# Optimization experiments

Hardware: AMD Instinct MI355X
Metric: run time of the kernel (lower is better)

The kernel has to match this reference:

```python
import jax, jax.numpy as jnp
import numpy as np

N_NODES = 50000
N_EDGES = 800000
NUM_GRAPHS = 256
F_IN = 64        # num_features (per-head out dim == in dim in this module)
HEADS = 4        # n_heads1
OUT_DIM = 128    # output_dim
HC = HEADS * F_IN
NEG_SLOPE = 0.2  # GATConv leaky_relu slope
EPS = 1e-5       # GraphNorm eps


def setup_inputs() -> dict:
    key = jax.random.key(0)
    ks = jax.random.split(key, 12)
    s = lambda k, shape, fan: (jax.random.normal(k, shape, jnp.float32) / np.sqrt(fan).astype(np.float32))
    return {
        "x": jax.random.normal(ks[0], (N_NODES, F_IN), jnp.float32),
        "edge_index": jax.random.randint(ks[1], (2, N_EDGES), 0, N_NODES),
        "batch": jnp.sort(jax.random.randint(ks[2], (N_NODES,), 0, NUM_GRAPHS)),
        # GATConv params
        "lin_w": s(ks[3], (HC, F_IN), F_IN),
        "att_src": s(ks[4], (HEADS, F_IN), F_IN),
        "att_dst": s(ks[5], (HEADS, F_IN), F_IN),
        "gat_bias": jnp.zeros((HC,), jnp.float32),
        # GraphNorm params
        "gn_weight": jnp.ones((HC,), jnp.float32),
        "gn_bias": jnp.zeros((HC,), jnp.float32),
        "gn_mean_scale": jnp.ones((HC,), jnp.float32),
        # fc_g1 / out heads
        "fc1_w": s(ks[6], (OUT_DIM, HC), HC), "fc1_b": jnp.zeros((OUT_DIM,), jnp.float32),
        "out_w": s(ks[7], (1, OUT_DIM), OUT_DIM), "out_b": jnp.zeros((1,), jnp.float32),
        # GlobalAttention gate_nn: Linear(HC,16) -> ReLU -> Linear(16,1) -> Sigmoid
        "att1_w": s(ks[8], (16, HC), HC), "att1_b": jnp.zeros((16,), jnp.float32),
        "att2_w": s(ks[9], (1, 16), 16), "att2_b": jnp.zeros((1,), jnp.float32),
    }


def _gat_conv(x, edge_index, lin_w, att_src, att_dst, gat_bias):
    """PyG GATConv with add_self_loops=True, concat heads. Returns (out [N,HC], alpha [E+N,H])."""
    N = x.shape[0]
    xh = (x @ lin_w.T).reshape(N, HEADS, F_IN)                 # [N,H,C]
    a_src = (xh * att_src[None]).sum(-1)                        # [N,H]
    a_dst = (xh * att_dst[None]).sum(-1)                        # [N,H]
    loops = jnp.arange(N)
    src = jnp.concatenate([edge_index[0], loops])               # [E+N]
    dst = jnp.concatenate([edge_index[1], loops])
    alpha = jax.nn.leaky_relu(a_src[src] + a_dst[dst], NEG_SLOPE)  # [E+N,H]
    # segment softmax over incoming edges of each dst node (self-loops guarantee non-empty)
    amax = jax.ops.segment_max(alpha, dst, num_segments=N)
    alpha = jnp.exp(alpha - amax[dst])
    denom = jax.ops.segment_sum(alpha, dst, num_segments=N)
    alpha = alpha / (denom[dst] + 1e-16)
    msg = xh[src] * alpha[:, :, None]                           # [E+N,H,C]
    out = jax.ops.segment_sum(msg, dst, num_segments=N).reshape(N, HC) + gat_bias
    return out, alpha


def _graph_norm(x, batch, weight, bias, mean_scale):
    ones = jnp.ones((x.shape[0],), x.dtype)
    cnt = jnp.maximum(jax.ops.segment_sum(ones, batch, num_segments=NUM_GRAPHS), 1.0)[:, None]
    mean = jax.ops.segment_sum(x, batch, num_segments=NUM_GRAPHS) / cnt
    sub = x - mean[batch] * mean_scale
    var = jax.ops.segment_sum(sub * sub, batch, num_segments=NUM_GRAPHS) / cnt
    return weight * sub / jnp.sqrt(var + EPS)[batch] + bias


def _global_attention(x, batch, att1_w, att1_b, att2_w, att2_b):
    gate = jax.nn.sigmoid(jax.nn.relu(x @ att1_w.T + att1_b) @ att2_w.T + att2_b)  # [N,1]
    gmax = jax.ops.segment_max(gate, batch, num_segments=NUM_GRAPHS)
    gate = jnp.exp(gate - gmax[batch])
    gden = jax.ops.segment_sum(gate, batch, num_segments=NUM_GRAPHS)
    gate = gate / (gden[batch] + 1e-16)
    return jax.ops.segment_sum(gate * x, batch, num_segments=NUM_GRAPHS)  # [G,HC]


def reference(x, edge_index, batch, lin_w, att_src, att_dst, gat_bias,
              gn_weight, gn_bias, gn_mean_scale, fc1_w, fc1_b, out_w, out_b,
              att1_w, att1_b, att2_w, att2_b):
    x2, alpha = _gat_conv(x, edge_index, lin_w, att_src, att_dst, gat_bias)
    h = _graph_norm(x2, batch, gn_weight, gn_bias, gn_mean_scale)
    h = jax.nn.relu(h)                                # node_dropout = identity (eval)
    pooled = _global_attention(h, batch, att1_w, att1_b, att2_w, att2_b)
    h = jax.nn.relu(pooled @ fc1_w.T + fc1_b)          # dropout = identity (eval)
    out = jax.nn.sigmoid(h @ out_w.T + out_b)          # [G,1]
    return out, alpha
```

## Files before the change

kernel.cpp:

```cpp
#include <hip/hip_runtime.h>
#include <hip/hip_fp16.h>
#include <math.h>

#define NN 50000
#define NE 800000
#define NG 256
#define NEG_SLOPE 0.2f
#define GEPS 1e-5f
#define CHUNK 64
#define NB 196
#define CAP 6144
#define NAB 196
#define EPB 4096
#define SPLIT 8
#define NLINB 782
#define ABLK 3321
#define GMAX 512

typedef _Float16 f16x8 __attribute__((ext_vector_type(8)));
typedef _Float16 f16x4 __attribute__((ext_vector_type(4)));
typedef float f32x4 __attribute__((ext_vector_type(4)));
typedef float f32x2 __attribute__((ext_vector_type(2)));

__device__ __forceinline__ float lrelu(float v){ return v > 0.f ? v : NEG_SLOPE * v; }

__global__ __launch_bounds__(256) void k_misc(const float* __restrict__ lin_w,
                                              _Float16* __restrict__ wh,
                                              const float* __restrict__ att1_w,
                                              _Float16* __restrict__ a1w,
                                              const int* __restrict__ batch,
                                              int* __restrict__ goff,
                                              int* __restrict__ gcnt,
                                              int* __restrict__ bucket_cnt) {
  int b = blockIdx.x, tid = threadIdx.x;
  if (b == 0) {
    if (tid < NB) bucket_cnt[tid] = 0;
    int g = tid;
    int lo = 0, hi = NN;
    while (lo < hi) { int mid = (lo + hi) >> 1; if (batch[mid] < g) lo = mid + 1; else hi = mid; }
    int start = lo;
    lo = 0; hi = NN;
    while (lo < hi) { int mid = (lo + hi) >> 1; if (batch[mid] < g + 1) lo = mid + 1; else hi = mid; }
    goff[g] = start;
    gcnt[g] = lo - start;
  } else if (b <= 16) {
    int i0 = (b - 1) * 1024 + tid * 4;
    float4 f = *(const float4*)&lin_w[i0];
    f16x4 h4;
    h4[0] = (_Float16)f.x; h4[1] = (_Float16)f.y; h4[2] = (_Float16)f.z; h4[3] = (_Float16)f.w;
    *(f16x4*)&wh[i0] = h4;
  } else {
    int i0 = (b - 17) * 1024 + tid * 4;
    float4 f = *(const float4*)&att1_w[i0];
    f16x4 h4;
    h4[0] = (_Float16)f.x; h4[1] = (_Float16)f.y; h4[2] = (_Float16)f.z; h4[3] = (_Float16)f.w;
    *(f16x4*)&a1w[i0] = h4;
  }
}

__device__ __forceinline__ void lin_body(char* smem,
                                         const float* __restrict__ x,
                                         const _Float16* __restrict__ wh,
                                         const float* __restrict__ att_src,
                                         const float* __restrict__ att_dst,
                                         unsigned char* __restrict__ xh8,
                                         float* __restrict__ a_src_n,
                                         float* __restrict__ a_dst_n) {
  unsigned char* s_f8 = (unsigned char*)smem;
  int w = threadIdx.x >> 6, lane = threadIdx.x & 63;
  int nb = blockIdx.x * 64 + w * 16;
  if (nb >= NN) return;
  int am = lane & 15, quad = lane >> 4;
  int wb = w * 4096;

  const float* xr = x + (size_t)(nb + am) * 64 + quad * 8;
  float4 f0 = *(const float4*)(xr);
  float4 f1 = *(const float4*)(xr + 4);
  float4 f2 = *(const float4*)(xr + 32);
  float4 f3 = *(const float4*)(xr + 36);
  f16x8 a0, a1;
  a0[0] = (_Float16)f0.x; a0[1] = (_Float16)f0.y; a0[2] = (_Float16)f0.z; a0[3] = (_Float16)f0.w;
  a0[4] = (_Float16)f1.x; a0[5] = (_Float16)f1.y; a0[6] = (_Float16)f1.z; a0[7] = (_Float16)f1.w;
  a1[0] = (_Float16)f2.x; a1[1] = (_Float16)f2.y; a1[2] = (_Float16)f2.z; a1[3] = (_Float16)f2.w;
  a1[4] = (_Float16)f3.x; a1[5] = (_Float16)f3.y; a1[6] = (_Float16)f3.z; a1[7] = (_Float16)f3.w;

  f32x4 acc[16];
#pragma unroll
  for (int ct = 0; ct < 16; ct++) acc[ct] = (f32x4){0.f, 0.f, 0.f, 0.f};

#pragma unroll
  for (int ct = 0; ct < 16; ct++) {
    const _Float16* wbp = wh + (size_t)(ct * 16 + am) * 64 + quad * 8;
    f16x8 b0 = *(const f16x8*)(wbp);
    f16x8 b1 = *(const f16x8*)(wbp + 32);
    acc[ct] = __builtin_amdgcn_mfma_f32_16x16x32_f16(a0, b0, acc[ct], 0, 0, 0);
    acc[ct] = __builtin_amdgcn_mfma_f32_16x16x32_f16(a1, b1, acc[ct], 0, 0, 0);
  }

  float ps[4][4], pd[4][4];
#pragma unroll
  for (int r = 0; r < 4; r++)
#pragma unroll
    for (int h = 0; h < 4; h++) { ps[r][h] = 0.f; pd[r][h] = 0.f; }
#pragma unroll
  for (int ct = 0; ct < 16; ct++) {
    int c = ct * 16 + am;
    float av = att_src[c];
    float dv = att_dst[c];
    int h = ct >> 2;
#pragma unroll
    for (int r = 0; r < 4; r++) {
      float v = acc[ct][r];
      ps[r][h] += v * av;
      pd[r][h] += v * dv;
    }
  }
#pragma unroll
  for (int r = 0; r < 4; r++)
#pragma unroll
    for (int h = 0; h < 4; h++) {
      float s = ps[r][h], d = pd[r][h];
#pragma unroll
      for (int o = 1; o < 16; o <<= 1) {
        s += __shfl_xor(s, o, 64);
        d += __shfl_xor(d, o, 64);
      }
      if (am == 0) {
        int node = nb + quad * 4 + r;
        a_src_n[node * 4 + h] = s;
        a_dst_n[node * 4 + h] = d;
      }
    }

#pragma unroll
  for (int r = 0; r < 4; r++) {
    uint4 u;
    int t;
    t = __builtin_amdgcn_cvt_pk_fp8_f32(acc[0][r],  acc[1][r],  0, 0);
    t = __builtin_amdgcn_cvt_pk_fp8_f32(acc[2][r],  acc[3][r],  t, 1);
    u.x = (unsigned)t;
    t = __builtin_amdgcn_cvt_pk_fp8_f32(acc[4][r],  acc[5][r],  0, 0);
    t = __builtin_amdgcn_cvt_pk_fp8_f32(acc[6][r],  acc[7][r],  t, 1);
    u.y = (unsigned)t;
    t = __builtin_amdgcn_cvt_pk_fp8_f32(acc[8][r],  acc[9][r],  0, 0);
    t = __builtin_amdgcn_cvt_pk_fp8_f32(acc[10][r], acc[11][r], t, 1);
    u.z = (unsigned)t;
    t = __builtin_amdgcn_cvt_pk_fp8_f32(acc[12][r], acc[13][r], 0, 0);
    t = __builtin_amdgcn_cvt_pk_fp8_f32(acc[14][r], acc[15][r], t, 1);
    u.w = (unsigned)t;
    *(uint4*)&s_f8[wb + (quad * 4 + r) * 256 + am * 16] = u;
  }
#pragma unroll
  for (int p = 0; p < 4; p++) {
    uint4 u = *(const uint4*)&s_f8[wb + p * 1024 + lane * 16];
    *(uint4*)&xh8[(size_t)nb * 256 + p * 1024 + lane * 16] = u;
  }
}

__device__ __forceinline__ void binA_body(char* smem, int b,
                                          const int* __restrict__ ei,
                                          int* __restrict__ bucket_cnt,
                                          int2* __restrict__ ebuf) {
  int2* sorted = (int2*)smem;
  int*  hist   = (int*)(smem + 32768);
  int*  lbase  = (int*)(smem + 33552);
  int*  cur    = (int*)(smem + 34336);
  int*  runb   = (int*)(smem + 35120);
  int*  wsum   = (int*)(smem + 35904);
  int tid = threadIdx.x, lane = tid & 63, wid = tid >> 6;
  int e0 = b * EPB, e1 = min(e0 + EPB, NE);
  int n = e1 - e0;
  bool full = (e0 + EPB <= NE);

  int dd[16];
  if (full) {
#pragma unroll
    for (int r = 0; r < 4; r++) {
      int e = e0 + r * 1024 + tid * 4;
      int4 v = *(const int4*)&ei[NE + e];
      dd[r * 4 + 0] = v.x; dd[r * 4 + 1] = v.y;
      dd[r * 4 + 2] = v.z; dd[r * 4 + 3] = v.w;
    }
  } else {
#pragma unroll
    for (int r = 0; r < 4; r++)
#pragma unroll
      for (int k = 0; k < 4; k++) {
        int e = e0 + r * 1024 + tid * 4 + k;
        dd[r * 4 + k] = (e < e1) ? ei[NE + e] : -1;
      }
  }
  for (int i = tid; i < NB; i += 256) hist[i] = 0;
  __syncthreads();
#pragma unroll
  for (int q = 0; q < 16; q++)
    if (dd[q] >= 0) atomicAdd(&hist[dd[q] >> 8], 1);
  __syncthreads();
  {
    int v = (tid < NB) ? hist[tid] : 0;
    int s = v;
#pragma unroll
    for (int o = 1; o < 64; o <<= 1) { int t = __shfl_up(s, o, 64); if (lane >= o) s += t; }
    if (lane == 63) wsum[wid] = s;
    __syncthreads();
    int wbase = 0;
    for (int k = 0; k < wid; k++) wbase += wsum[k];
    if (tid < NB) {
      int ex = wbase + s - v;
      lbase[tid] = ex;
      cur[tid] = ex;
      runb[tid] = atomicAdd(&bucket_cnt[tid], v);
    }
  }
  __syncthreads();
  int ss[16];
  if (full) {
#pragma unroll
    for (int r = 0; r < 4; r++) {
      int e = e0 + r * 1024 + tid * 4;
      int4 v = *(const int4*)&ei[e];
      ss[r * 4 + 0] = v.x; ss[r * 4 + 1] = v.y;
      ss[r * 4 + 2] = v.z; ss[r * 4 + 3] = v.w;
    }
  } else {
#pragma unroll
    for (int r = 0; r < 4; r++)
#pragma unroll
      for (int k = 0; k < 4; k++) {
        int e = e0 + r * 1024 + tid * 4 + k;
        ss[r * 4 + k] = (e < e1) ? ei[e] : 0;
      }
  }
#pragma unroll
  for (int q = 0; q < 16; q++) {
    int d = dd[q];
    if (d >= 0) {
      int lp = atomicAdd(&cur[d >> 8], 1);
      sorted[lp] = make_int2(d, ss[q]);
    }
  }
  __syncthreads();
  for (int i = tid; i < n; i += 256) {
    int2 e = sorted[i];
    int bk = e.x >> 8;
    int slot = runb[bk] + (i - lbase[bk]);
    if (slot < CAP) ebuf[(size_t)bk * CAP + slot] = e;
  }
}

__global__ __launch_bounds__(256) void k_linbin(const float* __restrict__ x,
                                                const _Float16* __restrict__ wh,
                                                const float* __restrict__ att_src,
                                                const float* __restrict__ att_dst,
                                                unsigned char* __restrict__ xh8,
                                                float* __restrict__ a_src_n,
                                                float* __restrict__ a_dst_n,
                                                const int* __restrict__ ei,
                                                int* __restrict__ bucket_cnt,
                                                int2* __restrict__ ebuf) {
  __shared__ __align__(16) char smem[35920];
  if (blockIdx.x < NLINB)
    lin_body(smem, x, wh, att_src, att_dst, xh8, a_src_n, a_dst_n);
  else
    binA_body(smem, blockIdx.x - NLINB, ei, bucket_cnt, ebuf);
}

__global__ __launch_bounds__(256) void k_binB(const int2* __restrict__ ebuf,
                                              const int* __restrict__ bucket_cnt,
                                              int* __restrict__ deg,
                                              int* __restrict__ offs,
                                              int* __restrict__ src_list) {
  __shared__ int hist[256];
  __shared__ int cur[256];
  __shared__ int wsum[4];
  __shared__ int bbase[NB];
  int b = blockIdx.x, tid = threadIdx.x, lane = tid & 63, wid = tid >> 6;
  {
    int v = (tid < NB) ? min(bucket_cnt[tid], CAP) : 0;
    int s = v;
#pragma unroll
    for (int o = 1; o < 64; o <<= 1) { int t = __shfl_up(s, o, 64); if (lane >= o) s += t; }
    if (lane == 63) wsum[wid] = s;
    __syncthreads();
    int wbase = 0;
    for (int k = 0; k < wid; k++) wbase += wsum[k];
    if (tid < NB) bbase[tid] = wbase + s - v;
  }
  __syncthreads();
  int cnt = min(bucket_cnt[b], CAP);
  int base = bbase[b];
  const int2* seg = ebuf + (size_t)b * CAP;
  hist[tid] = 0;
  __syncthreads();
  for (int i = tid; i < cnt; i += 256) atomicAdd(&hist[seg[i].x & 255], 1);
  __syncthreads();
  int v = hist[tid];
  int s = v;
#pragma unroll
  for (int o = 1; o < 64; o <<= 1) { int t = __shfl_up(s, o, 64); if (lane >= o) s += t; }
  if (lane == 63) wsum[wid] = s;
  __syncthreads();
  int wbase = 0;
  for (int k = 0; k < wid; k++) wbase += wsum[k];
  int excl = wbase + s - v;
  int node = b * 256 + tid;
  if (node < NN) {
    deg[node] = v;
    offs[node] = base + excl;
  }
  cur[tid] = excl;
  __syncthreads();
  for (int i = tid; i < cnt; i += 256) {
    int2 e = seg[i];
    int pos = base + atomicAdd(&cur[e.x & 255], 1);
    src_list[pos] = e.y;
  }
}

__global__ __launch_bounds__(64) void k_gat(const unsigned char* __restrict__ xh8,
                                            const float* __restrict__ a_src_n,
                                            const float* __restrict__ a_dst_n,
                                            const int* __restrict__ offs,
                                            const int* __restrict__ deg_arr,
                                            const int* __restrict__ src_list,
                                            const float* __restrict__ gat_bias,
                                            __half* __restrict__ x2h,
                                            float* __restrict__ den_inv) {
  __shared__ __align__(16) float s_al[CHUNK * 4];
  __shared__ int s_src[CHUNK];
  __shared__ __half s_tr[256];
  int n = blockIdx.x, lane = threadIdx.x;
  int off = offs[n], dg = deg_arr[n], cnt = dg + 1;
  float4 ad = *(const float4*)&a_dst_n[n * 4];
  int h = lane & 3;
  unsigned loff = 4u * (unsigned)lane;
  float acc0 = 0.f, acc1 = 0.f, acc2 = 0.f, acc3 = 0.f;

  if (cnt <= 64) {
    float e0 = 0.f, e1 = 0.f, e2 = 0.f, e3 = 0.f;
    if (lane < cnt) {
      int src = (lane < dg) ? src_list[off + lane] : n;
      float4 as = *(const float4*)&a_src_n[src * 4];
      e0 = __expf(lrelu(as.x + ad.x));
      e1 = __expf(lrelu(as.y + ad.y));
      e2 = __expf(lrelu(as.z + ad.z));
      e3 = __expf(lrelu(as.w + ad.w));
      s_src[lane] = src;
    }
    float s0 = e0, s1 = e1, s2 = e2, s3 = e3;
#pragma unroll
    for (int o = 32; o >= 1; o >>= 1) {
      s0 += __shfl_xor(s0, o, 64);
      s1 += __shfl_xor(s1, o, 64);
      s2 += __shfl_xor(s2, o, 64);
      s3 += __shfl_xor(s3, o, 64);
    }
    float i0 = 1.f / (s0 + 1e-16f), i1 = 1.f / (s1 + 1e-16f);
    float i2 = 1.f / (s2 + 1e-16f), i3 = 1.f / (s3 + 1e-16f);
    if (lane == 0) *(float4*)&den_inv[n * 4] = make_float4(i0, i1, i2, i3);
    if (lane < cnt) {
      s_al[lane * 4 + 0] = e0 * i0;
      s_al[lane * 4 + 1] = e1 * i1;
      s_al[lane * 4 + 2] = e2 * i2;
      s_al[lane * 4 + 3] = e3 * i3;
    }
    __syncthreads();
    int j = 0;
    for (; j + 4 <= cnt; j += 4) {
      unsigned oA = ((unsigned)s_src[j] << 8) + loff;
      unsigned oB = ((unsigned)s_src[j + 1] << 8) + loff;
      unsigned oC = ((unsigned)s_src[j + 2] << 8) + loff;
      unsigned oD = ((unsigned)s_src[j + 3] << 8) + loff;
      unsigned rA = *(const unsigned*)&xh8[oA];
      unsigned rB = *(const unsigned*)&xh8[oB];
      unsigned rC = *(const unsigned*)&xh8[oC];
      unsigned rD = *(const unsigned*)&xh8[oD];
      float aA = s_al[j * 4 + h], aB = s_al[(j + 1) * 4 + h];
      float aC = s_al[(j + 2) * 4 + h], aD = s_al[(j + 3) * 4 + h];
      f32x2 lA = __builtin_amdgcn_cvt_pk_f32_fp8((int)rA, 0);
      f32x2 hA = __builtin_amdgcn_cvt_pk_f32_fp8((int)rA, 1);
      f32x2 lB = __builtin_amdgcn_cvt_pk_f32_fp8((int)rB, 0);
      f32x2 hB = __builtin_amdgcn_cvt_pk_f32_fp8((int)rB, 1);
      f32x2 lC = __builtin_amdgcn_cvt_pk_f32_fp8((int)rC, 0);
      f32x2 hC = __builtin_amdgcn_cvt_pk_f32_fp8((int)rC, 1);
      f32x2 lD = __builtin_amdgcn_cvt_pk_f32_fp8((int)rD, 0);
      f32x2 hD = __builtin_amdgcn_cvt_pk_f32_fp8((int)rD, 1);
      acc0 += aA * lA[0] + aB * lB[0] + aC * lC[0] + aD * lD[0];
      acc1 += aA * lA[1] + aB * lB[1] + aC * lC[1] + aD * lD[1];
      acc2 += aA * hA[0] + aB * hB[0] + aC * hC[0] + aD * hD[0];
      acc3 += aA * hA[1] + aB * hB[1] + aC * hC[1] + aD * hD[1];
    }
    for (; j < cnt; j++) {
      unsigned oA = ((unsigned)s_src[j] << 8) + loff;
      unsigned rA = *(const unsigned*)&xh8[oA];
      float aA = s_al[j * 4 + h];
      f32x2 lA = __builtin_amdgcn_cvt_pk_f32_fp8((int)rA, 0);
      f32x2 hA = __builtin_amdgcn_cvt_pk_f32_fp8((int)rA, 1);
      acc0 += aA * lA[0];
      acc1 += aA * lA[1];
      acc2 += aA * hA[0];
      acc3 += aA * hA[1];
    }
  } else {
    float s0 = 0.f, s1 = 0.f, s2 = 0.f, s3 = 0.f;
    for (int j = lane; j < cnt; j += 64) {
      int src = (j < dg) ? src_list[off + j] : n;
      float4 as = *(const float4*)&a_src_n[src * 4];
      s0 += __expf(lrelu(as.x + ad.x));
      s1 += __expf(lrelu(as.y + ad.y));
      s2 += __expf(lrelu(as.z + ad.z));
      s3 += __expf(lrelu(as.w + ad.w));
    }
#pragma unroll
    for (int o = 32; o >= 1; o >>= 1) {
      s0 += __shfl_xor(s0, o, 64);
      s1 += __shfl_xor(s1, o, 64);
      s2 += __shfl_xor(s2, o, 64);
      s3 += __shfl_xor(s3, o, 64);
    }
    float i0 = 1.f / (s0 + 1e-16f), i1 = 1.f / (s1 + 1e-16f);
    float i2 = 1.f / (s2 + 1e-16f), i3 = 1.f / (s3 + 1e-16f);
    if (lane == 0) *(float4*)&den_inv[n * 4] = make_float4(i0, i1, i2, i3);
    for (int cb = 0; cb < cnt; cb += CHUNK) {
      int clen = min(CHUNK, cnt - cb);
      for (int j = lane; j < clen; j += 64) {
        int jj = cb + j;
        int src = (jj < dg) ? src_list[off + jj] : n;
        float4 as = *(const float4*)&a_src_n[src * 4];
        s_src[j] = src;
        s_al[j * 4 + 0] = __expf(lrelu(as.x + ad.x)) * i0;
        s_al[j * 4 + 1] = __expf(lrelu(as.y + ad.y)) * i1;
        s_al[j * 4 + 2] = __expf(lrelu(as.z + ad.z)) * i2;
        s_al[j * 4 + 3] = __expf(lrelu(as.w + ad.w)) * i3;
      }
      __syncthreads();
      for (int j = 0; j < clen; j++) {
        unsigned oA = ((unsigned)s_src[j] << 8) + loff;
        unsigned rA = *(const unsigned*)&xh8[oA];
        float aA = s_al[j * 4 + h];
        f32x2 lA = __builtin_amdgcn_cvt_pk_f32_fp8((int)rA, 0);
        f32x2 hA = __builtin_amdgcn_cvt_pk_f32_fp8((int)rA, 1);
        acc0 += aA * lA[0];
        acc1 += aA * lA[1];
        acc2 += aA * hA[0];
        acc3 += aA * hA[1];
      }
      __syncthreads();
    }
  }

  int cb0 = (lane & 3) * 64 + (lane >> 2);
  s_tr[cb0 +  0] = __float2half(acc0 + gat_bias[cb0 +  0]);
  s_tr[cb0 + 16] = __float2half(acc1 + gat_bias[cb0 + 16]);
  s_tr[cb0 + 32] = __float2half(acc2 + gat_bias[cb0 + 32]);
  s_tr[cb0 + 48] = __float2half(acc3 + gat_bias[cb0 + 48]);
  __syncthreads();
  uint2 u = *(const uint2*)&s_tr[4 * lane];
  *(uint2*)&x2h[(size_t)n * 256 + 4 * lane] = u;
}

__global__ __launch_bounds__(256) void k_alst(const int* __restrict__ ei,
                                              const float* __restrict__ a_src_n,
                                              const float* __restrict__ a_dst_n,
                                              const float* __restrict__ den_inv,
                                              float* __restrict__ alpha_out,
                                              const __half* __restrict__ x2h,
                                              const int* __restrict__ gcnt,
                                              const int* __restrict__ goff,
                                              float* __restrict__ psumA,
                                              float* __restrict__ psumB) {
  if (blockIdx.x < ABLK) {
    int idx = blockIdx.x * 256 + threadIdx.x;
    if (idx >= NE + NN) return;
    int s, d;
    if (idx < NE) { s = ei[idx]; d = ei[NE + idx]; }
    else          { s = idx - NE; d = s; }
    float4 as = *(const float4*)&a_src_n[s * 4];
    float4 ad = *(const float4*)&a_dst_n[d * 4];
    float4 iv = *(const float4*)&den_inv[d * 4];
    float4 a;
    a.x = __expf(lrelu(as.x + ad.x)) * iv.x;
    a.y = __expf(lrelu(as.y + ad.y)) * iv.y;
    a.z = __expf(lrelu(as.z + ad.z)) * iv.z;
    a.w = __expf(lrelu(as.w + ad.w)) * iv.w;
    *(float4*)&alpha_out[(size_t)idx * 4] = a;
  } else {
    int b = blockIdx.x - ABLK, c = threadIdx.x;
    int g = b >> 3, s = b & 7;
    int cnt = gcnt[g], start = goff[g];
    const __half* p = x2h + (size_t)start * 256 + c;
    float sum = 0.f, sum2 = 0.f;
    int i = s;
    for (; i + 56 < cnt; i += 64) {
      float v0 = __half2float(p[(size_t)(i +  0) * 256]);
      float v1 = __half2float(p[(size_t)(i +  8) * 256]);
      float v2 = __half2float(p[(size_t)(i + 16) * 256]);
      float v3 = __half2float(p[(size_t)(i + 24) * 256]);
      float v4 = __half2float(p[(size_t)(i + 32) * 256]);
      float v5 = __half2float(p[(size_t)(i + 40) * 256]);
      float v6 = __half2float(p[(size_t)(i + 48) * 256]);
      float v7 = __half2float(p[(size_t)(i + 56) * 256]);
      sum += ((v0 + v1) + (v2 + v3)) + ((v4 + v5) + (v6 + v7));
      sum2 += ((v0 * v0 + v1 * v1) + (v2 * v2 + v3 * v3)) +
              ((v4 * v4 + v5 * v5) + (v6 * v6 + v7 * v7));
    }
    for (; i < cnt; i += 8) { float v = __half2float(p[(size_t)i * 256]); sum += v; sum2 += v * v; }
    psumA[b * 256 + c] = sum;
    psumB[b * 256 + c] = sum2;
  }
}

__global__ __launch_bounds__(256) void k_tail(const float* __restrict__ psumA,
                                              const float* __restrict__ psumB,
                                              const int* __restrict__ gcnt,
                                              const int* __restrict__ goff,
                                              const float* __restrict__ gn_w,
                                              const float* __restrict__ gn_b,
                                              const float* __restrict__ gn_ms,
                                              const __half* __restrict__ x2h,
                                              const _Float16* __restrict__ a1w,
                                              const float* __restrict__ att1_b,
                                              const float* __restrict__ att2_w,
                                              const float* __restrict__ att2_b,
                                              const float* __restrict__ fc1_w,
                                              const float* __restrict__ fc1_b,
                                              const float* __restrict__ out_w,
                                              const float* __restrict__ out_b,
                                              float* __restrict__ outp) {
  __shared__ __align__(16) float s_sc[256];
  __shared__ __align__(16) float s_sh[256];
  __shared__ float s_gate[GMAX];
  __shared__ __align__(16) float pool_s[256];
  __shared__ float hred[128];
  __shared__ float red[4];
  int g = blockIdx.x, tid = threadIdx.x, lane = tid & 63, wid = tid >> 6;
  int cnt = gcnt[g], start = goff[g];

  {
    int b0 = g * SPLIT, c = tid;
    float S = 0.f, S2 = 0.f;
#pragma unroll
    for (int k = 0; k < SPLIT; k++) {
      S  += psumA[(b0 + k) * 256 + c];
      S2 += psumB[(b0 + k) * 256 + c];
    }
    float fc = fmaxf((float)cnt, 1.f);
    float mean = S / fc;
    float mm = mean * gn_ms[c];
    float var = fmaxf(S2 / fc - 2.f * mm * mean + mm * mm, 0.f);
    float sc = gn_w[c] / sqrtf(var + GEPS);
    s_sc[c] = sc;
    s_sh[c] = gn_b[c] - sc * mm;
  }
  __syncthreads();

  int am = lane & 15, quad = lane >> 4;
  float b1 = att1_b[am], w2 = att2_w[am], b2 = att2_b[0];
  const _Float16* bp = a1w + am * 256 + quad * 8;
  for (int i0 = wid * 16; i0 < cnt; i0 += 64) {
    int node = start + i0 + am;
    if (node > NN - 1) node = NN - 1;
    const __half* xp = x2h + (size_t)node * 256 + quad * 8;
    f32x4 ga = (f32x4){0.f, 0.f, 0.f, 0.f};
#pragma unroll
    for (int kb = 0; kb < 8; kb++) {
      f16x8 xv = *(const f16x8*)(xp + kb * 32);
      int cb = quad * 8 + kb * 32;
      float4 sc0 = *(const float4*)&s_sc[cb];
      float4 sc1 = *(const float4*)&s_sc[cb + 4];
      float4 sh0 = *(const float4*)&s_sh[cb];
      float4 sh1 = *(const float4*)&s_sh[cb + 4];
      f16x8 a;
      a[0] = (_Float16)fmaxf(sc0.x * (float)xv[0] + sh0.x, 0.f);
      a[1] = (_Float16)fmaxf(sc0.y * (float)xv[1] + sh0.y, 0.f);
      a[2] = (_Float16)fmaxf(sc0.z * (float)xv[2] + sh0.z, 0.f);
      a[3] = (_Float16)fmaxf(sc0.w * (float)xv[3] + sh0.w, 0.f);
      a[4] = (_Float16)fmaxf(sc1.x * (float)xv[4] + sh1.x, 0.f);
      a[5] = (_Float16)fmaxf(sc1.y * (float)xv[5] + sh1.y, 0.f);
      a[6] = (_Float16)fmaxf(sc1.z * (float)xv[6] + sh1.z, 0.f);
      a[7] = (_Float16)fmaxf(sc1.w * (float)xv[7] + sh1.w, 0.f);
      f16x8 b = *(const f16x8*)(bp + kb * 32);
      ga = __builtin_amdgcn_mfma_f32_16x16x32_f16(a, b, ga, 0, 0, 0);
    }
#pragma unroll
    for (int r = 0; r < 4; r++) {
      float t = w2 * fmaxf(ga[r] + b1, 0.f);
#pragma unroll
      for (int o = 1; o < 16; o <<= 1) t += __shfl_xor(t, o, 64);
      if (am == 0) {
        int li = i0 + quad * 4 + r;
        if (li < cnt && li < GMAX)
          s_gate[li] = __expf(1.f / (1.f + __expf(-(t + b2))));
      }
    }
  }
  __syncthreads();

  float ls = 0.f;
  for (int i = tid; i < cnt; i += 256) ls += s_gate[i];
#pragma unroll
  for (int o = 32; o >= 1; o >>= 1) ls += __shfl_xor(ls, o, 64);
  if (lane == 0) red[wid] = ls;
  __syncthreads();
  float rden = 1.f / (red[0] + red[1] + red[2] + red[3] + 1e-16f);

  {
    int c = tid;
    float sc = s_sc[c], sh = s_sh[c];
    const __half* p = x2h + (size_t)start * 256 + c;
    float a0 = 0.f, a1_ = 0.f, a2 = 0.f, a3 = 0.f;
    float a4 = 0.f, a5 = 0.f, a6 = 0.f, a7 = 0.f;
    int i = 0;
    for (; i + 7 < cnt; i += 8) {
      float v0 = __half2float(p[(size_t)(i + 0) * 256]);
      float v1 = __half2float(p[(size_t)(i + 1) * 256]);
      float v2 = __half2float(p[(size_t)(i + 2) * 256]);
      float v3 = __half2float(p[(size_t)(i + 3) * 256]);
      float v4 = __half2float(p[(size_t)(i + 4) * 256]);
      float v5 = __half2float(p[(size_t)(i + 5) * 256]);
      float v6 = __half2float(p[(size_t)(i + 6) * 256]);
      float v7 = __half2float(p[(size_t)(i + 7) * 256]);
      a0 += s_gate[i + 0] * fmaxf(sc * v0 + sh, 0.f);
      a1_ += s_gate[i + 1] * fmaxf(sc * v1 + sh, 0.f);
      a2 += s_gate[i + 2] * fmaxf(sc * v2 + sh, 0.f);
      a3 += s_gate[i + 3] * fmaxf(sc * v3 + sh, 0.f);
      a4 += s_gate[i + 4] * fmaxf(sc * v4 + sh, 0.f);
      a5 += s_gate[i + 5] * fmaxf(sc * v5 + sh, 0.f);
      a6 += s_gate[i + 6] * fmaxf(sc * v6 + sh, 0.f);
      a7 += s_gate[i + 7] * fmaxf(sc * v7 + sh, 0.f);
    }
    for (; i < cnt; i++)
      a0 += s_gate[i] * fmaxf(sc * __half2float(p[(size_t)i * 256]) + sh, 0.f);
    pool_s[c] = ((((a0 + a1_) + (a2 + a3)) + ((a4 + a5) + (a6 + a7)))) * rden;
  }
  __syncthreads();

  float4 psv = *(const float4*)&pool_s[4 * lane];
  for (int j0 = 0; j0 < 32; j0++) {
    int j = wid * 32 + j0;
    float4 w = *(const float4*)&fc1_w[j * 256 + 4 * lane];
    float d = w.x * psv.x + w.y * psv.y + w.z * psv.z + w.w * psv.w;
#pragma unroll
    for (int o = 32; o >= 1; o >>= 1) d += __shfl_xor(d, o, 64);
    if (lane == 0) hred[j] = fmaxf(d + fc1_b[j], 0.f) * out_w[j];
  }
  __syncthreads();
  if (tid < 128) {
    float v = hred[tid];
#pragma unroll
    for (int o = 32; o >= 1; o >>= 1) v += __shfl_xor(v, o, 64);
    if (lane == 0) red[wid] = v;
  }
  __syncthreads();
  if (tid == 0) outp[g] = 1.f / (1.f + __expf(-(red[0] + red[1] + out_b[0])));
}

extern "C" void kernel_launch(void* const* d_in, const int* in_sizes, int n_in,
                              void* d_out, int out_size, void* d_ws, size_t ws_size,
                              hipStream_t stream) {
  const float* x        = (const float*)d_in[0];
  const int*   ei       = (const int*)d_in[1];
  const int*   batch    = (const int*)d_in[2];
  const float* lin_w    = (const float*)d_in[3];
  const float* att_src  = (const float*)d_in[4];
  const float* att_dst  = (const float*)d_in[5];
  const float* gat_bias = (const float*)d_in[6];
  const float* gn_w     = (const float*)d_in[7];
  const float* gn_b     = (const float*)d_in[8];
  const float* gn_ms    = (const float*)d_in[9];
  const float* fc1_w    = (const float*)d_in[10];
  const float* fc1_b    = (const float*)d_in[11];
  const float* out_w    = (const float*)d_in[12];
  const float* out_b    = (const float*)d_in[13];
  const float* att1_w   = (const float*)d_in[14];
  const float* att1_b   = (const float*)d_in[15];
  const float* att2_w   = (const float*)d_in[16];
  const float* att2_b   = (const float*)d_in[17];

  float* outp  = (float*)d_out;
  float* alpha = outp + NG;

  char* wsb = (char*)d_ws;
  size_t o = 0;
  auto A = [&](size_t bytes) -> char* {
    char* p = wsb + o;
    o += (bytes + 255) & ~(size_t)255;
    return p;
  };
  unsigned char* xh8 = (unsigned char*)A((size_t)NN * 256);
  __half*   x2h      = (__half*)A((size_t)NN * 256 * 2);
  _Float16* wh       = (_Float16*)A((size_t)256 * 64 * 2);
  _Float16* a1w      = (_Float16*)A((size_t)16 * 256 * 2);
  float* a_src_n  = (float*)A((size_t)NN * 4 * 4);
  float* a_dst_n  = (float*)A((size_t)NN * 4 * 4);
  float* den_inv  = (float*)A((size_t)NN * 4 * 4);
  float* psumA    = (float*)A((size_t)NG * SPLIT * 256 * 4);
  float* psumB    = (float*)A((size_t)NG * SPLIT * 256 * 4);
  int*   deg      = (int*)A((size_t)NN * 4);
  int*   gcnt     = (int*)A((size_t)NG * 4);
  int*   offs     = (int*)A((size_t)NN * 4);
  int*   goff     = (int*)A((size_t)NG * 4);
  int*   src_list = (int*)A((size_t)NE * 4);
  int2*  ebuf     = (int2*)A((size_t)NB * CAP * 8);
  int*   bucket_cnt  = (int*)A((size_t)NB * 4);

  k_misc<<<21, 256, 0, stream>>>(lin_w, wh, att1_w, a1w, batch, goff, gcnt, bucket_cnt);
  k_linbin<<<NLINB + NAB, 256, 0, stream>>>(x, wh, att_src, att_dst, xh8, a_src_n, a_dst_n,
                                            ei, bucket_cnt, ebuf);
  k_binB<<<NB, 256, 0, stream>>>(ebuf, bucket_cnt, deg, offs, src_list);
  k_gat<<<NN, 64, 0, stream>>>(xh8, a_src_n, a_dst_n, offs, deg, src_list,
                               gat_bias, x2h, den_inv);
  k_alst<<<ABLK + NG * SPLIT, 256, 0, stream>>>(ei, a_src_n, a_dst_n, den_inv, alpha,
                                                x2h, gcnt, goff, psumA, psumB);
  k_tail<<<NG, 256, 0, stream>>>(psumA, psumB, gcnt, goff, gn_w, gn_b, gn_ms, x2h,
                                 a1w, att1_b, att2_w, att2_b, fc1_w, fc1_b,
                                 out_w, out_b, outp);
}
```

Measured before the change: 233.8 us.

## Fuse alpha and GraphNorm stats into tail kernel, shrink edge-binning blocks

The separate alpha/partial-stats kernel is removed. Alpha computation now runs as extra blocks of the tail kernel, and each graph's tail block computes its own GraphNorm sum and sum-of-squares directly from x2h, no longer reading split partial sums. This drops one kernel launch and the psum round trip, but the per-graph statistics pass becomes serial within a single block. Separately, edge binning uses smaller chunks (3072 edges) over more blocks, which cuts shared memory per block.

```diff
diff --git a/kernel.cpp b/kernel.cpp
--- a/kernel.cpp
+++ b/kernel.cpp
@@ -10,9 +10,8 @@
 #define CHUNK 64
 #define NB 196
 #define CAP 6144
-#define NAB 196
-#define EPB 4096
-#define SPLIT 8
+#define NAB 261
+#define EPB 3072
 #define NLINB 782
 #define ABLK 3321
 #define GMAX 512
@@ -162,20 +161,20 @@
                                           int* __restrict__ bucket_cnt,
                                           int2* __restrict__ ebuf) {
   int2* sorted = (int2*)smem;
-  int*  hist   = (int*)(smem + 32768);
-  int*  lbase  = (int*)(smem + 33552);
-  int*  cur    = (int*)(smem + 34336);
-  int*  runb   = (int*)(smem + 35120);
-  int*  wsum   = (int*)(smem + 35904);
+  int*  hist   = (int*)(smem + 24576);
+  int*  lbase  = (int*)(smem + 25360);
+  int*  cur    = (int*)(smem + 26144);
+  int*  runb   = (int*)(smem + 26928);
+  int*  wsum   = (int*)(smem + 27712);
   int tid = threadIdx.x, lane = tid & 63, wid = tid >> 6;
   int e0 = b * EPB, e1 = min(e0 + EPB, NE);
   int n = e1 - e0;
   bool full = (e0 + EPB <= NE);
 
-  int dd[16];
+  int dd[12];
   if (full) {
 #pragma unroll
-    for (int r = 0; r < 4; r++) {
+    for (int r = 0; r < 3; r++) {
       int e = e0 + r * 1024 + tid * 4;
       int4 v = *(const int4*)&ei[NE + e];
       dd[r * 4 + 0] = v.x; dd[r * 4 + 1] = v.y;
@@ -183,17 +182,17 @@
     }
   } else {
 #pragma unroll
-    for (int r = 0; r < 4; r++)
+    for (int r = 0; r < 3; r++)
 #pragma unroll
       for (int k = 0; k < 4; k++) {
         int e = e0 + r * 1024 + tid * 4 + k;
         dd[r * 4 + k] = (e < e1) ? ei[NE + e] : -1;
       }
   }
-  for (int i = tid; i < NB; i += 256) hist[i] = 0;
-  __syncthreads();
-#pragma unroll
-  for (int q = 0; q < 16; q++)
+  if (tid < NB) hist[tid] = 0;
+  __syncthreads();
+#pragma unroll
+  for (int q = 0; q < 12; q++)
     if (dd[q] >= 0) atomicAdd(&hist[dd[q] >> 8], 1);
   __syncthreads();
   {
@@ -213,10 +212,10 @@
     }
   }
   __syncthreads();
-  int ss[16];
+  int ss[12];
   if (full) {
 #pragma unroll
-    for (int r = 0; r < 4; r++) {
+    for (int r = 0; r < 3; r++) {
       int e = e0 + r * 1024 + tid * 4;
       int4 v = *(const int4*)&ei[e];
       ss[r * 4 + 0] = v.x; ss[r * 4 + 1] = v.y;
@@ -224,7 +223,7 @@
     }
   } else {
 #pragma unroll
-    for (int r = 0; r < 4; r++)
+    for (int r = 0; r < 3; r++)
 #pragma unroll
       for (int k = 0; k < 4; k++) {
         int e = e0 + r * 1024 + tid * 4 + k;
@@ -232,7 +231,7 @@
       }
   }
 #pragma unroll
-  for (int q = 0; q < 16; q++) {
+  for (int q = 0; q < 12; q++) {
     int d = dd[q];
     if (d >= 0) {
       int lp = atomicAdd(&cur[d >> 8], 1);
@@ -258,7 +257,7 @@
                                                 const int* __restrict__ ei,
                                                 int* __restrict__ bucket_cnt,
                                                 int2* __restrict__ ebuf) {
-  __shared__ __align__(16) char smem[35920];
+  __shared__ __align__(16) char smem[27744];
   if (blockIdx.x < NLINB)
     lin_body(smem, x, wh, att_src, att_dst, xh8, a_src_n, a_dst_n);
   else
@@ -459,59 +458,11 @@
   *(uint2*)&x2h[(size_t)n * 256 + 4 * lane] = u;
 }
 
-__global__ __launch_bounds__(256) void k_alst(const int* __restrict__ ei,
+__global__ __launch_bounds__(256) void k_tail(const int* __restrict__ ei,
                                               const float* __restrict__ a_src_n,
                                               const float* __restrict__ a_dst_n,
                                               const float* __restrict__ den_inv,
                                               float* __restrict__ alpha_out,
-                                              const __half* __restrict__ x2h,
-                                              const int* __restrict__ gcnt,
-                                              const int* __restrict__ goff,
-                                              float* __restrict__ psumA,
-                                              float* __restrict__ psumB) {
-  if (blockIdx.x < ABLK) {
-    int idx = blockIdx.x * 256 + threadIdx.x;
-    if (idx >= NE + NN) return;
-    int s, d;
-    if (idx < NE) { s = ei[idx]; d = ei[NE + idx]; }
-    else          { s = idx - NE; d = s; }
-    float4 as = *(const float4*)&a_src_n[s * 4];
-    float4 ad = *(const float4*)&a_dst_n[d * 4];
-    float4 iv = *(const float4*)&den_inv[d * 4];
-    float4 a;
-    a.x = __expf(lrelu(as.x + ad.x)) * iv.x;
-    a.y = __expf(lrelu(as.y + ad.y)) * iv.y;
-    a.z = __expf(lrelu(as.z + ad.z)) * iv.z;
-    a.w = __expf(lrelu(as.w + ad.w)) * iv.w;
-    *(float4*)&alpha_out[(size_t)idx * 4] = a;
-  } else {
-    int b = blockIdx.x - ABLK, c = threadIdx.x;
-    int g = b >> 3, s = b & 7;
-    int cnt = gcnt[g], start = goff[g];
-    const __half* p = x2h + (size_t)start * 256 + c;
-    float sum = 0.f, sum2 = 0.f;
-    int i = s;
-    for (; i + 56 < cnt; i += 64) {
-      float v0 = __half2float(p[(size_t)(i +  0) * 256]);
-      float v1 = __half2float(p[(size_t)(i +  8) * 256]);
-      float v2 = __half2float(p[(size_t)(i + 16) * 256]);
-      float v3 = __half2float(p[(size_t)(i + 24) * 256]);
-      float v4 = __half2float(p[(size_t)(i + 32) * 256]);
-      float v5 = __half2float(p[(size_t)(i + 40) * 256]);
-      float v6 = __half2float(p[(size_t)(i + 48) * 256]);
-      float v7 = __half2float(p[(size_t)(i + 56) * 256]);
-      sum += ((v0 + v1) + (v2 + v3)) + ((v4 + v5) + (v6 + v7));
-      sum2 += ((v0 * v0 + v1 * v1) + (v2 * v2 + v3 * v3)) +
-              ((v4 * v4 + v5 * v5) + (v6 * v6 + v7 * v7));
-    }
-    for (; i < cnt; i += 8) { float v = __half2float(p[(size_t)i * 256]); sum += v; sum2 += v * v; }
-    psumA[b * 256 + c] = sum;
-    psumB[b * 256 + c] = sum2;
-  }
-}
-
-__global__ __launch_bounds__(256) void k_tail(const float* __restrict__ psumA,
-                                              const float* __restrict__ psumB,
                                               const int* __restrict__ gcnt,
                                               const int* __restrict__ goff,
                                               const float* __restrict__ gn_w,
@@ -527,6 +478,24 @@
                                               const float* __restrict__ out_w,
                                               const float* __restrict__ out_b,
                                               float* __restrict__ outp) {
+  if (blockIdx.x >= NG) {
+    int idx = (blockIdx.x - NG) * 256 + threadIdx.x;
+    if (idx >= NE + NN) return;
+    int s, d;
+    if (idx < NE) { s = ei[idx]; d = ei[NE + idx]; }
+    else          { s = idx - NE; d = s; }
+    float4 as = *(const float4*)&a_src_n[s * 4];
+    float4 ad = *(const float4*)&a_dst_n[d * 4];
+    float4 iv = *(const float4*)&den_inv[d * 4];
+    float4 a;
+    a.x = __expf(lrelu(as.x + ad.x)) * iv.x;
+    a.y = __expf(lrelu(as.y + ad.y)) * iv.y;
+    a.z = __expf(lrelu(as.z + ad.z)) * iv.z;
+    a.w = __expf(lrelu(as.w + ad.w)) * iv.w;
+    *(float4*)&alpha_out[(size_t)idx * 4] = a;
+    return;
+  }
+
   __shared__ __align__(16) float s_sc[256];
   __shared__ __align__(16) float s_sh[256];
   __shared__ float s_gate[GMAX];
@@ -537,13 +506,24 @@
   int cnt = gcnt[g], start = goff[g];
 
   {
-    int b0 = g * SPLIT, c = tid;
+    int c = tid;
+    const __half* p = x2h + (size_t)start * 256 + c;
     float S = 0.f, S2 = 0.f;
-#pragma unroll
-    for (int k = 0; k < SPLIT; k++) {
-      S  += psumA[(b0 + k) * 256 + c];
-      S2 += psumB[(b0 + k) * 256 + c];
-    }
+    int i = 0;
+    for (; i + 7 < cnt; i += 8) {
+      float v0 = __half2float(p[(size_t)(i + 0) * 256]);
+      float v1 = __half2float(p[(size_t)(i + 1) * 256]);
+      float v2 = __half2float(p[(size_t)(i + 2) * 256]);
+      float v3 = __half2float(p[(size_t)(i + 3) * 256]);
+      float v4 = __half2float(p[(size_t)(i + 4) * 256]);
+      float v5 = __half2float(p[(size_t)(i + 5) * 256]);
+      float v6 = __half2float(p[(size_t)(i + 6) * 256]);
+      float v7 = __half2float(p[(size_t)(i + 7) * 256]);
+      S  += ((v0 + v1) + (v2 + v3)) + ((v4 + v5) + (v6 + v7));
+      S2 += ((v0 * v0 + v1 * v1) + (v2 * v2 + v3 * v3)) +
+            ((v4 * v4 + v5 * v5) + (v6 * v6 + v7 * v7));
+    }
+    for (; i < cnt; i++) { float v = __half2float(p[(size_t)i * 256]); S += v; S2 += v * v; }
     float fc = fmaxf((float)cnt, 1.f);
     float mean = S / fc;
     float mm = mean * gn_ms[c];
@@ -694,8 +674,6 @@
   float* a_src_n  = (float*)A((size_t)NN * 4 * 4);
   float* a_dst_n  = (float*)A((size_t)NN * 4 * 4);
   float* den_inv  = (float*)A((size_t)NN * 4 * 4);
-  float* psumA    = (float*)A((size_t)NG * SPLIT * 256 * 4);
-  float* psumB    = (float*)A((size_t)NG * SPLIT * 256 * 4);
   int*   deg      = (int*)A((size_t)NN * 4);
   int*   gcnt     = (int*)A((size_t)NG * 4);
   int*   offs     = (int*)A((size_t)NN * 4);
@@ -710,9 +688,8 @@
   k_binB<<<NB, 256, 0, stream>>>(ebuf, bucket_cnt, deg, offs, src_list);
   k_gat<<<NN, 64, 0, stream>>>(xh8, a_src_n, a_dst_n, offs, deg, src_list,
                                gat_bias, x2h, den_inv);
-  k_alst<<<ABLK + NG * SPLIT, 256, 0, stream>>>(ei, a_src_n, a_dst_n, den_inv, alpha,
-                                                x2h, gcnt, goff, psumA, psumB);
-  k_tail<<<NG, 256, 0, stream>>>(psumA, psumB, gcnt, goff, gn_w, gn_b, gn_ms, x2h,
-                                 a1w, att1_b, att2_w, att2_b, fc1_w, fc1_b,
-                                 out_w, out_b, outp);
-}
+  k_tail<<<NG + ABLK, 256, 0, stream>>>(ei, a_src_n, a_dst_n, den_inv, alpha,
+                                        gcnt, goff, gn_w, gn_b, gn_ms, x2h,
+                                        a1w, att1_b, att2_w, att2_b, fc1_w, fc1_b,
+                                        out_w, out_b, outp);
+}
```

Result: no change. 234.7 us (+0.4%).
